# Performance work log

Measured on AMD Instinct MI355X. Metric: run time of the kernel, lower is better.

The kernel has to match this reference:

```python
import jax, jax.numpy as jnp
import numpy as np

N = 50000      # nodes
E = 800000     # edges
D_IN = 128
D_H = 256
D_OUT = 128
EPS = 1e-5
SLOPE = 0.01   # LeakyReLU negative_slope


def setup_inputs() -> dict:
    key = jax.random.key(0)
    ks = jax.random.split(key, 24)
    inp = {}
    inp["x"] = jax.random.normal(ks[0], (N, D_IN), dtype=jnp.float32)
    inp["edge_index"] = jax.random.randint(ks[1], (2, E), 0, N, dtype=jnp.int32)
    dims = [(D_IN, D_H), (D_H, D_H), (D_H, D_H), (D_H, D_OUT)]
    for i, (di, do) in enumerate(dims, start=1):
        inp[f"W{i}"] = jax.random.normal(ks[4 * i - 2], (di, do), dtype=jnp.float32) / np.float32(np.sqrt(di))
        inp[f"b{i}"] = jnp.zeros((do,), dtype=jnp.float32)
        inp[f"g{i}"] = 1.0 + 0.1 * jax.random.normal(ks[4 * i - 1], (do,), dtype=jnp.float32)   # BN gamma
        inp[f"be{i}"] = 0.1 * jax.random.normal(ks[4 * i], (do,), dtype=jnp.float32)            # BN beta
    inp["ln_g"] = 1.0 + 0.1 * jax.random.normal(ks[18], (D_OUT,), dtype=jnp.float32)
    inp["ln_b"] = 0.1 * jax.random.normal(ks[19], (D_OUT,), dtype=jnp.float32)
    return inp


def _gcn_conv(x, W, b, src, dst, nisq):
    # PyG GCNConv: linear first, then sym-normalized aggregation with self-loops.
    xl = x @ W                                   # [N, do]
    coef = (nisq[src] * nisq[dst])[:, None]      # [E, 1]
    msg = xl[src] * coef                         # [E, do] gather
    agg = jax.ops.segment_sum(msg, dst, num_segments=N)  # scatter-add
    # self-loop contribution: deg^{-1/2}_i * deg^{-1/2}_i * xl_i
    return agg + xl * (nisq * nisq)[:, None] + b


def _bn(x, g, b):
    # BatchNorm1d, training-mode batch statistics (biased variance)
    m = jnp.mean(x, axis=0)
    v = jnp.var(x, axis=0)
    return (x - m) * jax.lax.rsqrt(v + EPS) * g + b


def _lrelu(x):
    return jnp.where(x >= 0, x, SLOPE * x)


def _layer_norm(x, g, b):
    m = jnp.mean(x, axis=-1, keepdims=True)
    v = jnp.var(x, axis=-1, keepdims=True)
    return (x - m) * jax.lax.rsqrt(v + EPS) * g + b


def reference(x, edge_index, W1, b1, g1, be1, W2, b2, g2, be2, W3, b3, g3, be3, W4, b4, g4, be4, ln_g, ln_b):
    src = edge_index[0]
    dst = edge_index[1]
    # degrees with self-loops (computed once, shared by all 4 convs)
    deg = jax.ops.segment_sum(jnp.ones((E,), dtype=x.dtype), dst, num_segments=N) + 1.0
    nisq = jax.lax.rsqrt(deg)  # deg >= 1 so safe

    identity = x  # input_dim == output_dim -> residual_fc is Identity
    h = _lrelu(_bn(_gcn_conv(x, W1, b1, src, dst, nisq), g1, be1))   # dropout = identity (eval)
    h = _lrelu(_bn(_gcn_conv(h, W2, b2, src, dst, nisq), g2, be2))
    h = _lrelu(_bn(_gcn_conv(h, W3, b3, src, dst, nisq), g3, be3))
    h = _gcn_conv(h, W4, b4, src, dst, nisq)
    h = h + identity
    return _layer_norm(_bn(h, g4, be4), ln_g, ln_b)
```

## Files before the change

kernel.cpp:

```cpp
#include <hip/hip_runtime.h>

#define N_NODES 50000
#define NPAD 50176
#define N_EDGES 800000
#define EPS_C 1e-5f
#define SLOPE_C 0.01f

typedef __attribute__((ext_vector_type(8))) short short8v;
typedef __attribute__((ext_vector_type(4))) float f32x4;

__device__ __forceinline__ unsigned short f2bf(float f) {
  unsigned u = __float_as_uint(f);
  u += 0x7fffu + ((u >> 16) & 1u);
  return (unsigned short)(u >> 16);
}
__device__ __forceinline__ unsigned packbf(float a, float b) {
  return (unsigned)f2bf(a) | ((unsigned)f2bf(b) << 16);
}
__device__ __forceinline__ float bflo(unsigned u) { return __uint_as_float(u << 16); }
__device__ __forceinline__ float bfhi(unsigned u) { return __uint_as_float(u & 0xffff0000u); }

__device__ __forceinline__ void gload16(const unsigned short* g, unsigned short* l) {
  __builtin_amdgcn_global_load_lds(
      (const __attribute__((address_space(1))) unsigned int*)g,
      (__attribute__((address_space(3))) unsigned int*)l, 16, 0, 0);
}

#define HGRID 3125
__global__ void hist_wcast_kernel(const int* __restrict__ dst, int* __restrict__ hist,
                                  const float* __restrict__ W1, const float* __restrict__ W2,
                                  const float* __restrict__ W3, const float* __restrict__ W4,
                                  unsigned short* __restrict__ Wt1, unsigned short* __restrict__ Wt2,
                                  unsigned short* __restrict__ Wt3, unsigned short* __restrict__ Wt4) {
  const int b = blockIdx.x;
  if (b < HGRID) {
    const int e = b * 256 + threadIdx.x;
    if (e < N_EDGES) atomicAdd(&hist[dst[e]], 1);
    return;
  }
  const int w = (b - HGRID) * 256 + threadIdx.x;
  if (w < 32768) {
    Wt1[(size_t)(w & 255) * 128 + (w >> 8)] = f2bf(W1[w]);
  } else if (w < 98304) {
    const int v = w - 32768;
    Wt2[(size_t)(v & 255) * 256 + (v >> 8)] = f2bf(W2[v]);
  } else if (w < 163840) {
    const int v = w - 98304;
    Wt3[(size_t)(v & 255) * 256 + (v >> 8)] = f2bf(W3[v]);
  } else {
    const int v = w - 163840;
    Wt4[(size_t)(v & 127) * 256 + (v >> 7)] = f2bf(W4[v]);
  }
}

__global__ __launch_bounds__(1024) void scan1_kernel(
    const int* __restrict__ hist, int* __restrict__ off, int* __restrict__ partial,
    float* __restrict__ nisq, int n) {
  __shared__ int tmp[1024];
  const int tid = threadIdx.x;
  const int i = blockIdx.x * 1024 + tid;
  const int v = (i < n) ? hist[i] : 0;
  tmp[tid] = v;
  __syncthreads();
  int x = v;
  for (int o = 1; o < 1024; o <<= 1) {
    const int y = (tid >= o) ? tmp[tid - o] : 0;
    __syncthreads();
    x += y;
    tmp[tid] = x;
    __syncthreads();
  }
  if (i < n) {
    off[i] = x - v;
    nisq[i] = rsqrtf((float)v + 1.0f);
  }
  if (tid == 1023) partial[blockIdx.x] = x;
}

#define SGRID 196
#define NBCH 49
__global__ void scan3f_kernel(int* __restrict__ off, int* __restrict__ cursor,
                              const int* __restrict__ partial,
                              const float* __restrict__ nisq, const float* __restrict__ x,
                              unsigned short* __restrict__ xs) {
  const int b = blockIdx.x;
  if (b < SGRID) {
    const int i = b * 256 + threadIdx.x;
    const int chunk = b >> 2;
    int pre = 0;
    for (int k = 0; k < chunk; ++k) pre += partial[k];
    if (i < N_NODES) {
      const int o = off[i] + pre;
      off[i] = o;
      cursor[i] = o;
    }
    if (b == SGRID - 1 && threadIdx.x == 0)
      off[N_NODES] = pre + partial[NBCH - 1];
    return;
  }
  const int idx = (b - SGRID) * 256 + threadIdx.x;
  if (idx >= N_NODES * 32) return;
  const int row = idx >> 5;
  const int c = (idx & 31) * 4;
  const float s = nisq[row];
  const float4 v = *reinterpret_cast<const float4*>(&x[(size_t)row * 128 + c]);
  ushort4 o;
  o.x = f2bf(v.x * s); o.y = f2bf(v.y * s);
  o.z = f2bf(v.z * s); o.w = f2bf(v.w * s);
  *reinterpret_cast<ushort4*>(&xs[(size_t)row * 128 + c]) = o;
}

__global__ void scatter_kernel(const int* __restrict__ src, const int* __restrict__ dst,
                               int* __restrict__ cursor, int* __restrict__ esorted, int E) {
  const int e = blockIdx.x * 256 + threadIdx.x;
  if (e < E) {
    const int p = atomicAdd(&cursor[dst[e]], 1);
    esorted[p] = src[e];
  }
}

template <int MODE, int KC, int NCOL_LOG2>
__global__ __launch_bounds__(256) void gemm2_kernel(
    const unsigned short* __restrict__ A, const unsigned short* __restrict__ Wt,
    const float* __restrict__ bias, unsigned short* __restrict__ Yb,
    float* __restrict__ colsum, float* __restrict__ colsumsq, int M) {
  __shared__ __align__(16) unsigned short Bs[64][KC];
  __shared__ __align__(16) unsigned short As[128][64];
  __shared__ float sred[2][64][2];
  const int tid = threadIdx.x;
  const int lane = tid & 63;
  const int wave = tid >> 6;
  const int wr = wave >> 1, wc = wave & 1;
  const int chunkN = gridDim.x >> 3;
  const int swz = (blockIdx.x & 7) * chunkN + (blockIdx.x >> 3);
  const int row0 = (swz >> NCOL_LOG2) * 128;
  const int col0 = (swz & ((1 << NCOL_LOG2) - 1)) * 64;
  const int l15 = lane & 15;
  const int lhi = lane >> 4;

  constexpr int CPR = KC / 8;
  constexpr int BITER = 64 * CPR / 256;
#pragma unroll
  for (int c = 0; c < BITER; ++c) {
    const int ch = c * 256 + tid;
    const int rb = ch / CPR;
    const int cb = ch % CPR;
    const short8v v =
        *reinterpret_cast<const short8v*>(&Wt[(size_t)(col0 + rb) * KC + cb * 8]);
    *reinterpret_cast<short8v*>(&Bs[rb][(cb ^ (rb & 7)) * 8]) = v;
  }

  f32x4 acc[4][2];
#pragma unroll
  for (int i = 0; i < 4; ++i)
#pragma unroll
    for (int j = 0; j < 2; ++j) acc[i][j] = (f32x4){0.f, 0.f, 0.f, 0.f};

  for (int k0 = 0; k0 < KC; k0 += 64) {
    __syncthreads();
#pragma unroll
    for (int c = 0; c < 4; ++c) {
      const int chunk = (c * 4 + wave) * 64 + lane;
      const int r = chunk >> 3;
      const int cksrc = (chunk & 7) ^ (r & 7);
      gload16(&A[(size_t)(row0 + r) * KC + k0 + cksrc * 8], &As[0][0] + chunk * 8);
    }
    __syncthreads();
    short8v bfr[2][2];
#pragma unroll
    for (int nr = 0; nr < 2; ++nr)
#pragma unroll
      for (int h = 0; h < 2; ++h) {
        const int rowb = wc * 32 + nr * 16 + l15;
        const int chb = (k0 >> 3) + h * 4 + lhi;
        bfr[nr][h] = *reinterpret_cast<const short8v*>(&Bs[rowb][(chb ^ (rowb & 7)) * 8]);
      }
#pragma unroll
    for (int mr = 0; mr < 4; ++mr) {
#pragma unroll
      for (int h = 0; h < 2; ++h) {
        const int rowa = wr * 64 + mr * 16 + l15;
        const int cha = (h * 4 + lhi) ^ (rowa & 7);
        const short8v af = *reinterpret_cast<const short8v*>(&As[rowa][cha * 8]);
#pragma unroll
        for (int nr = 0; nr < 2; ++nr)
          acc[mr][nr] = __builtin_amdgcn_mfma_f32_16x16x32_bf16(
              af, bfr[nr][h], acc[mr][nr], 0, 0, 0);
      }
    }
  }
  float bcol[2] = {0.f, 0.f};
  if constexpr (MODE == 1) {
#pragma unroll
    for (int nr = 0; nr < 2; ++nr) bcol[nr] = bias[col0 + wc * 32 + nr * 16 + l15];
  }
  float s_c[2] = {0.f, 0.f}, q_c[2] = {0.f, 0.f};
#pragma unroll
  for (int mr = 0; mr < 4; ++mr) {
#pragma unroll
    for (int r = 0; r < 4; ++r) {
      const int grow = row0 + wr * 64 + mr * 16 + lhi * 4 + r;
#pragma unroll
      for (int nr = 0; nr < 2; ++nr) {
        const int gcol = col0 + wc * 32 + nr * 16 + l15;
        const float v = acc[mr][nr][r] + bcol[nr];
        Yb[(size_t)grow * M + gcol] = f2bf(v);
        if constexpr (MODE == 1) {
          if (grow < N_NODES) {
            s_c[nr] += v;
            q_c[nr] += v * v;
          }
        }
      }
    }
  }
  if constexpr (MODE == 1) {
#pragma unroll
    for (int nr = 0; nr < 2; ++nr) {
      float s = s_c[nr], q = q_c[nr];
      s += __shfl_xor(s, 16, 64); q += __shfl_xor(q, 16, 64);
      s += __shfl_xor(s, 32, 64); q += __shfl_xor(q, 32, 64);
      if (lhi == 0) {
        const int cl = wc * 32 + nr * 16 + l15;
        sred[0][cl][wr] = s;
        sred[1][cl][wr] = q;
      }
    }
    __syncthreads();
    if (tid < 128) {
      const int which = tid >> 6;
      const int cl = tid & 63;
      const float tot = sred[which][cl][0] + sred[which][cl][1];
      float* dstp = which ? colsumsq : colsum;
      atomicAdd(&dstp[col0 + cl], tot);
    }
  }
}

template <int DO, bool ADD_BIAS, bool HAS_RES, bool OUT_BF16>
__global__ __launch_bounds__(256) void aggregate4_kernel(
    const unsigned short* __restrict__ Y, const int* __restrict__ segoff,
    const int* __restrict__ esorted, const float* __restrict__ nisq,
    const float* __restrict__ bias, const float* __restrict__ resid,
    void* __restrict__ Tv) {
  constexpr int V2 = DO / 32;
  const int wave = threadIdx.x >> 6;
  const int lane = threadIdx.x & 63;
  const int half = lane >> 5;
  const int l31 = lane & 31;
  const int n = blockIdx.x * 4 + wave;
  const int colbase = l31 * V2;
  if (n >= N_NODES) {
    if (half == 0) {
      if constexpr (OUT_BF16) {
        unsigned short* tr = (unsigned short*)Tv + (size_t)n * DO + colbase;
        if constexpr (V2 == 8) *reinterpret_cast<uint4*>(tr) = (uint4){0, 0, 0, 0};
        else *reinterpret_cast<uint2*>(tr) = (uint2){0, 0};
      } else {
        float* tr = (float*)Tv + (size_t)n * DO + colbase;
        if constexpr (V2 == 8) {
          *reinterpret_cast<float4*>(tr) = (float4){0.f, 0.f, 0.f, 0.f};
          *reinterpret_cast<float4*>(tr + 4) = (float4){0.f, 0.f, 0.f, 0.f};
        } else {
          *reinterpret_cast<float4*>(tr) = (float4){0.f, 0.f, 0.f, 0.f};
        }
      }
    }
    return;
  }
  const unsigned short* Yc = Y + colbase;
  float a0[V2], a1[V2];
#pragma unroll
  for (int i = 0; i < V2; ++i) { a0[i] = 0.f; a1[i] = 0.f; }
  const int s = segoff[n];
  const int e = segoff[n + 1];

  if constexpr (V2 == 8) {
    auto acc8 = [&](float* a, const uint4 v) {
      a[0] += bflo(v.x); a[1] += bfhi(v.x);
      a[2] += bflo(v.y); a[3] += bfhi(v.y);
      a[4] += bflo(v.z); a[5] += bfhi(v.z);
      a[6] += bflo(v.w); a[7] += bfhi(v.w);
    };
    int j = s + half;
    for (; j + 2 < e; j += 4) {
      const int i0 = esorted[j];
      const int i1 = esorted[j + 2];
      const uint4 v0 = *reinterpret_cast<const uint4*>(Yc + (size_t)i0 * DO);
      const uint4 v1 = *reinterpret_cast<const uint4*>(Yc + (size_t)i1 * DO);
      acc8(a0, v0); acc8(a1, v1);
    }
    if (j < e) acc8(a0, *reinterpret_cast<const uint4*>(Yc + (size_t)esorted[j] * DO));
    if (half == 0) acc8(a1, *reinterpret_cast<const uint4*>(Yc + (size_t)n * DO));
  } else {
    auto acc4 = [&](float* a, const uint2 v) {
      a[0] += bflo(v.x); a[1] += bfhi(v.x);
      a[2] += bflo(v.y); a[3] += bfhi(v.y);
    };
    int j = s + half;
    for (; j + 2 < e; j += 4) {
      const int i0 = esorted[j];
      const int i1 = esorted[j + 2];
      const uint2 v0 = *reinterpret_cast<const uint2*>(Yc + (size_t)i0 * DO);
      const uint2 v1 = *reinterpret_cast<const uint2*>(Yc + (size_t)i1 * DO);
      acc4(a0, v0); acc4(a1, v1);
    }
    if (j < e) acc4(a0, *reinterpret_cast<const uint2*>(Yc + (size_t)esorted[j] * DO));
    if (half == 0) acc4(a1, *reinterpret_cast<const uint2*>(Yc + (size_t)n * DO));
  }

  const float sc = nisq[n];
  float vals[V2];
#pragma unroll
  for (int i = 0; i < V2; ++i) {
    float t = a0[i] + a1[i];
    t += __shfl_xor(t, 32, 64);
    t *= sc;
    if (half == 0) {
      if (ADD_BIAS) t += bias[colbase + i];
      if (HAS_RES) t += resid[(size_t)n * DO + colbase + i];
    }
    vals[i] = t;
  }
  if (half == 0) {
    if constexpr (OUT_BF16) {
      unsigned short* tr = (unsigned short*)Tv + (size_t)n * DO + colbase;
      if constexpr (V2 == 8) {
        uint4 o;
        o.x = packbf(vals[0], vals[1]); o.y = packbf(vals[2], vals[3]);
        o.z = packbf(vals[4], vals[5]); o.w = packbf(vals[6], vals[7]);
        *reinterpret_cast<uint4*>(tr) = o;
      } else {
        uint2 o;
        o.x = packbf(vals[0], vals[1]); o.y = packbf(vals[2], vals[3]);
        *reinterpret_cast<uint2*>(tr) = o;
      }
    } else {
      float* tr = (float*)Tv + (size_t)n * DO + colbase;
      if constexpr (V2 == 8) {
        float4 o0 = {vals[0], vals[1], vals[2], vals[3]};
        float4 o1 = {vals[4], vals[5], vals[6], vals[7]};
        *reinterpret_cast<float4*>(tr) = o0;
        *reinterpret_cast<float4*>(tr + 4) = o1;
      } else {
        float4 o = {vals[0], vals[1], vals[2], vals[3]};
        *reinterpret_cast<float4*>(tr) = o;
      }
    }
  }
}

__global__ void stats_bf16_kernel(const unsigned short* __restrict__ T,
                                  float* __restrict__ colsum, float* __restrict__ colsumsq,
                                  int n, int rowsPerBlock) {
  const int t = threadIdx.x;
  const int c2 = t & 63;
  const int rh = t >> 6;
  const int r0 = blockIdx.x * rowsPerBlock;
  int r1 = r0 + rowsPerBlock;
  if (r1 > n) r1 = n;
  const unsigned* T32 = (const unsigned*)T;
  float s0 = 0.f, q0 = 0.f, s1 = 0.f, q1 = 0.f;
  for (int r = r0 + rh; r < r1; r += 2) {
    const unsigned v = T32[(size_t)r * 64 + c2];
    const float a = bflo(v), b = bfhi(v);
    s0 += a; q0 += a * a;
    s1 += b; q1 += b * b;
  }
  atomicAdd(&colsum[c2 * 2], s0);
  atomicAdd(&colsumsq[c2 * 2], q0);
  atomicAdd(&colsum[c2 * 2 + 1], s1);
  atomicAdd(&colsumsq[c2 * 2 + 1], q1);
}

__global__ void bn_lrelu_nisq_kernel(const unsigned short* __restrict__ Tb,
                                     const float* __restrict__ colsum,
                                     const float* __restrict__ colsumsq,
                                     const float* __restrict__ g, const float* __restrict__ be,
                                     const float* __restrict__ nisq,
                                     unsigned short* __restrict__ outb,
                                     size_t total8, float invN) {
  const size_t idx = (size_t)blockIdx.x * 256 + threadIdx.x;
  if (idx >= total8) return;
  const int row = (int)(idx >> 5);
  if (row >= N_NODES) {
    *reinterpret_cast<uint4*>(&outb[idx * 8]) = (uint4){0, 0, 0, 0};
    return;
  }
  const unsigned c = ((unsigned)idx & 31u) * 8;
  const float sc = nisq[row];
  uint4 v = *reinterpret_cast<const uint4*>(&Tb[idx * 8]);
  float z[8] = {bflo(v.x), bfhi(v.x), bflo(v.y), bfhi(v.y),
                bflo(v.z), bfhi(v.z), bflo(v.w), bfhi(v.w)};
  const float4 cs0 = *reinterpret_cast<const float4*>(&colsum[c]);
  const float4 cs1 = *reinterpret_cast<const float4*>(&colsum[c + 4]);
  const float4 cq0 = *reinterpret_cast<const float4*>(&colsumsq[c]);
  const float4 cq1 = *reinterpret_cast<const float4*>(&colsumsq[c + 4]);
  const float4 gv0 = *reinterpret_cast<const float4*>(&g[c]);
  const float4 gv1 = *reinterpret_cast<const float4*>(&g[c + 4]);
  const float4 bv0 = *reinterpret_cast<const float4*>(&be[c]);
  const float4 bv1 = *reinterpret_cast<const float4*>(&be[c + 4]);
  const float css[8] = {cs0.x, cs0.y, cs0.z, cs0.w, cs1.x, cs1.y, cs1.z, cs1.w};
  const float cqq[8] = {cq0.x, cq0.y, cq0.z, cq0.w, cq1.x, cq1.y, cq1.z, cq1.w};
  const float ggg[8] = {gv0.x, gv0.y, gv0.z, gv0.w, gv1.x, gv1.y, gv1.z, gv1.w};
  const float bbb[8] = {bv0.x, bv0.y, bv0.z, bv0.w, bv1.x, bv1.y, bv1.z, bv1.w};
#pragma unroll
  for (int k = 0; k < 8; ++k) {
    const float m = css[k] * invN;
    const float rs = rsqrtf(cqq[k] * invN - m * m + EPS_C);
    float zz = (z[k] - m) * rs * ggg[k] + bbb[k];
    zz = (zz >= 0.f) ? zz : SLOPE_C * zz;
    z[k] = zz * sc;
  }
  v.x = packbf(z[0], z[1]); v.y = packbf(z[2], z[3]);
  v.z = packbf(z[4], z[5]); v.w = packbf(z[6], z[7]);
  *reinterpret_cast<uint4*>(&outb[idx * 8]) = v;
}

__global__ __launch_bounds__(256) void bn_ln_kernel(
    const unsigned short* __restrict__ T, const float* __restrict__ colsum,
    const float* __restrict__ colsumsq, const float* __restrict__ g,
    const float* __restrict__ be, const float* __restrict__ lng,
    const float* __restrict__ lnb, float* __restrict__ out, float invN) {
  const int wave = threadIdx.x >> 6;
  const int lane = threadIdx.x & 63;
  const int n = blockIdx.x * 4 + wave;
  if (n >= N_NODES) return;
  const int c = lane * 2;
  const unsigned tv = *reinterpret_cast<const unsigned*>(&T[(size_t)n * 128 + c]);
  const float t0 = bflo(tv), t1 = bfhi(tv);
  float z[2];
#pragma unroll
  for (int k = 0; k < 2; ++k) {
    const float m = colsum[c + k] * invN;
    const float v = colsumsq[c + k] * invN - m * m;
    const float tvv = (k == 0) ? t0 : t1;
    z[k] = (tvv - m) * rsqrtf(v + EPS_C) * g[c + k] + be[c + k];
  }
  float s = z[0] + z[1];
  float q = z[0] * z[0] + z[1] * z[1];
  for (int o = 32; o > 0; o >>= 1) {
    s += __shfl_xor(s, o, 64);
    q += __shfl_xor(q, o, 64);
  }
  const float mean = s * (1.f / 128.f);
  const float var = q * (1.f / 128.f) - mean * mean;
  const float rs = rsqrtf(var + EPS_C);
  float2 o2;
  o2.x = (z[0] - mean) * rs * lng[c] + lnb[c];
  o2.y = (z[1] - mean) * rs * lng[c + 1] + lnb[c + 1];
  *reinterpret_cast<float2*>(&out[(size_t)n * 128 + c]) = o2;
}

extern "C" void kernel_launch(void* const* d_in, const int* in_sizes, int n_in,
                              void* d_out, int out_size, void* d_ws, size_t ws_size,
                              hipStream_t stream) {
  const float* x = (const float*)d_in[0];
  const int* ei = (const int*)d_in[1];
  const int* srcp = ei;
  const int* dstp = ei + N_EDGES;
  const float* W1 = (const float*)d_in[2];
  const float* b1 = (const float*)d_in[3];
  const float* g1 = (const float*)d_in[4];
  const float* be1 = (const float*)d_in[5];
  const float* W2 = (const float*)d_in[6];
  const float* b2 = (const float*)d_in[7];
  const float* g2 = (const float*)d_in[8];
  const float* be2 = (const float*)d_in[9];
  const float* W3 = (const float*)d_in[10];
  const float* b3 = (const float*)d_in[11];
  const float* g3 = (const float*)d_in[12];
  const float* be3 = (const float*)d_in[13];
  const float* W4 = (const float*)d_in[14];
  const float* b4 = (const float*)d_in[15];
  const float* g4 = (const float*)d_in[16];
  const float* be4 = (const float*)d_in[17];
  const float* lng = (const float*)d_in[18];
  const float* lnb = (const float*)d_in[19];
  float* out = (float*)d_out;

  char* ws = (char*)d_ws;
  size_t off_b = 0;
  auto alloc = [&](size_t bytes) -> void* {
    void* p = (void*)(ws + off_b);
    off_b += (bytes + 255) & ~(size_t)255;
    return p;
  };
  int* hist = (int*)alloc((size_t)N_NODES * 4);
  float* cs1 = (float*)alloc(256 * 4);
  float* cq1 = (float*)alloc(256 * 4);
  float* cs2 = (float*)alloc(256 * 4);
  float* cq2 = (float*)alloc(256 * 4);
  float* cs3 = (float*)alloc(256 * 4);
  float* cq3 = (float*)alloc(256 * 4);
  float* cs4 = (float*)alloc(256 * 4);
  float* cq4 = (float*)alloc(256 * 4);
  const size_t zero_bytes = off_b;
  int* segoff = (int*)alloc((size_t)(N_NODES + 1) * 4);
  int* cursor = (int*)alloc((size_t)N_NODES * 4);
  float* nisq = (float*)alloc((size_t)N_NODES * 4);
  int* esorted = (int*)alloc((size_t)N_EDGES * 4);
  int* partial = (int*)alloc(64 * 4);
  unsigned short* Wt1 = (unsigned short*)alloc((size_t)256 * 128 * 2);
  unsigned short* Wt2 = (unsigned short*)alloc((size_t)256 * 256 * 2);
  unsigned short* Wt3 = (unsigned short*)alloc((size_t)256 * 256 * 2);
  unsigned short* Wt4 = (unsigned short*)alloc((size_t)128 * 256 * 2);
  unsigned short* tblA = (unsigned short*)alloc((size_t)NPAD * 256 * 2);
  unsigned short* tblB = (unsigned short*)alloc((size_t)NPAD * 256 * 2);
  unsigned short* S = (unsigned short*)alloc((size_t)NPAD * 256 * 2);
  unsigned short* Tb = (unsigned short*)alloc((size_t)NPAD * 256 * 2);

  const float invN = 1.0f / (float)N_NODES;
  const int egrid = (N_EDGES + 255) / 256;
  const int aggrid = NPAD / 4;
  const int statgrid = (N_NODES + 127) / 128;
  const int mgrid256 = (NPAD / 128) * 4;
  const int mgrid128 = (NPAD / 128) * 2;
  const unsigned bngrid = (unsigned)(((size_t)NPAD * 32 + 255) / 256);

  hipMemsetAsync(hist, 0, zero_bytes, stream);

  hist_wcast_kernel<<<HGRID + 768, 256, 0, stream>>>(dstp, hist, W1, W2, W3, W4,
                                                     Wt1, Wt2, Wt3, Wt4);
  scan1_kernel<<<NBCH, 1024, 0, stream>>>(hist, segoff, partial, nisq, N_NODES);
  scan3f_kernel<<<SGRID + 6250, 256, 0, stream>>>(segoff, cursor, partial, nisq, x, tblA);
  scatter_kernel<<<egrid, 256, 0, stream>>>(srcp, dstp, cursor, esorted, N_EDGES);

  aggregate4_kernel<128, false, false, true><<<aggrid, 256, 0, stream>>>(
      tblA, segoff, esorted, nisq, nullptr, nullptr, S);
  gemm2_kernel<1, 128, 2><<<mgrid256, 256, 0, stream>>>(S, Wt1, b1, Tb, cs1, cq1, 256);
  bn_lrelu_nisq_kernel<<<bngrid, 256, 0, stream>>>(Tb, cs1, cq1, g1, be1, nisq,
                                                   tblB, (size_t)NPAD * 32, invN);

  aggregate4_kernel<256, false, false, true><<<aggrid, 256, 0, stream>>>(
      tblB, segoff, esorted, nisq, nullptr, nullptr, S);
  gemm2_kernel<1, 256, 2><<<mgrid256, 256, 0, stream>>>(S, Wt2, b2, Tb, cs2, cq2, 256);
  bn_lrelu_nisq_kernel<<<bngrid, 256, 0, stream>>>(Tb, cs2, cq2, g2, be2, nisq,
                                                   tblA, (size_t)NPAD * 32, invN);

  aggregate4_kernel<256, false, false, true><<<aggrid, 256, 0, stream>>>(
      tblA, segoff, esorted, nisq, nullptr, nullptr, S);
  gemm2_kernel<1, 256, 2><<<mgrid256, 256, 0, stream>>>(S, Wt3, b3, Tb, cs3, cq3, 256);
  bn_lrelu_nisq_kernel<<<bngrid, 256, 0, stream>>>(Tb, cs3, cq3, g3, be3, nisq,
                                                   tblB, (size_t)NPAD * 32, invN);

  gemm2_kernel<0, 256, 1><<<mgrid128, 256, 0, stream>>>(tblB, Wt4, nullptr, S,
                                                        nullptr, nullptr, 128);
  aggregate4_kernel<128, true, true, true><<<aggrid, 256, 0, stream>>>(
      S, segoff, esorted, nisq, b4, x, Tb);
  stats_bf16_kernel<<<statgrid, 128, 0, stream>>>(Tb, cs4, cq4, N_NODES, 128);
  bn_ln_kernel<<<(N_NODES + 3) / 4, 256, 0, stream>>>(Tb, cs4, cq4, g4, be4, lng, lnb, out, invN);
}
```

Before: 478.4 us.

## Widen GEMM tile to 128x128 and stream weight slices per k-step via LDS

The GEMM kernel's output tile grows from 128x64 to 128x128, so each wave computes a 64x64 sub-tile with 16 accumulators. Instead of preloading the whole weight panel into shared memory up front, the 64-wide k-slice of the weights is loaded asynchronously through global_load_lds alongside A each k-step. This halves the number of blocks and the redundant A-tile reads across column tiles. In exchange it uses more registers per thread, and the smaller grid (about 784 or 392 blocks) may fill the GPU's compute units less evenly.

```diff
diff --git a/kernel.cpp b/kernel.cpp
--- a/kernel.cpp
+++ b/kernel.cpp
@@ -120,13 +120,13 @@
 }
 
 template <int MODE, int KC, int NCOL_LOG2>
-__global__ __launch_bounds__(256) void gemm2_kernel(
+__global__ __launch_bounds__(256) void gemm4_kernel(
     const unsigned short* __restrict__ A, const unsigned short* __restrict__ Wt,
     const float* __restrict__ bias, unsigned short* __restrict__ Yb,
     float* __restrict__ colsum, float* __restrict__ colsumsq, int M) {
-  __shared__ __align__(16) unsigned short Bs[64][KC];
   __shared__ __align__(16) unsigned short As[128][64];
-  __shared__ float sred[2][64][2];
+  __shared__ __align__(16) unsigned short Bs[128][64];
+  __shared__ float sred[2][128][2];
   const int tid = threadIdx.x;
   const int lane = tid & 63;
   const int wave = tid >> 6;
@@ -134,27 +134,15 @@
   const int chunkN = gridDim.x >> 3;
   const int swz = (blockIdx.x & 7) * chunkN + (blockIdx.x >> 3);
   const int row0 = (swz >> NCOL_LOG2) * 128;
-  const int col0 = (swz & ((1 << NCOL_LOG2) - 1)) * 64;
+  const int col0 = (swz & ((1 << NCOL_LOG2) - 1)) * 128;
   const int l15 = lane & 15;
   const int lhi = lane >> 4;
 
-  constexpr int CPR = KC / 8;
-  constexpr int BITER = 64 * CPR / 256;
-#pragma unroll
-  for (int c = 0; c < BITER; ++c) {
-    const int ch = c * 256 + tid;
-    const int rb = ch / CPR;
-    const int cb = ch % CPR;
-    const short8v v =
-        *reinterpret_cast<const short8v*>(&Wt[(size_t)(col0 + rb) * KC + cb * 8]);
-    *reinterpret_cast<short8v*>(&Bs[rb][(cb ^ (rb & 7)) * 8]) = v;
-  }
-
-  f32x4 acc[4][2];
+  f32x4 acc[4][4];
 #pragma unroll
   for (int i = 0; i < 4; ++i)
 #pragma unroll
-    for (int j = 0; j < 2; ++j) acc[i][j] = (f32x4){0.f, 0.f, 0.f, 0.f};
+    for (int j = 0; j < 4; ++j) acc[i][j] = (f32x4){0.f, 0.f, 0.f, 0.f};
 
   for (int k0 = 0; k0 < KC; k0 += 64) {
     __syncthreads();
@@ -162,47 +150,52 @@
     for (int c = 0; c < 4; ++c) {
       const int chunk = (c * 4 + wave) * 64 + lane;
       const int r = chunk >> 3;
-      const int cksrc = (chunk & 7) ^ (r & 7);
-      gload16(&A[(size_t)(row0 + r) * KC + k0 + cksrc * 8], &As[0][0] + chunk * 8);
+      const int ck = (chunk & 7) ^ (r & 7);
+      gload16(&A[(size_t)(row0 + r) * KC + k0 + ck * 8], &As[0][0] + chunk * 8);
+    }
+#pragma unroll
+    for (int c = 0; c < 4; ++c) {
+      const int chunk = (c * 4 + wave) * 64 + lane;
+      const int r = chunk >> 3;
+      const int ck = (chunk & 7) ^ (r & 7);
+      gload16(&Wt[(size_t)(col0 + r) * KC + k0 + ck * 8], &Bs[0][0] + chunk * 8);
     }
     __syncthreads();
-    short8v bfr[2][2];
-#pragma unroll
-    for (int nr = 0; nr < 2; ++nr)
-#pragma unroll
-      for (int h = 0; h < 2; ++h) {
-        const int rowb = wc * 32 + nr * 16 + l15;
-        const int chb = (k0 >> 3) + h * 4 + lhi;
-        bfr[nr][h] = *reinterpret_cast<const short8v*>(&Bs[rowb][(chb ^ (rowb & 7)) * 8]);
-      }
-#pragma unroll
-    for (int mr = 0; mr < 4; ++mr) {
-#pragma unroll
-      for (int h = 0; h < 2; ++h) {
+#pragma unroll
+    for (int h = 0; h < 2; ++h) {
+      short8v bfr[4];
+#pragma unroll
+      for (int nr = 0; nr < 4; ++nr) {
+        const int rowb = wc * 64 + nr * 16 + l15;
+        const int chb = (h * 4 + lhi) ^ (rowb & 7);
+        bfr[nr] = *reinterpret_cast<const short8v*>(&Bs[rowb][chb * 8]);
+      }
+#pragma unroll
+      for (int mr = 0; mr < 4; ++mr) {
         const int rowa = wr * 64 + mr * 16 + l15;
         const int cha = (h * 4 + lhi) ^ (rowa & 7);
         const short8v af = *reinterpret_cast<const short8v*>(&As[rowa][cha * 8]);
 #pragma unroll
-        for (int nr = 0; nr < 2; ++nr)
+        for (int nr = 0; nr < 4; ++nr)
           acc[mr][nr] = __builtin_amdgcn_mfma_f32_16x16x32_bf16(
-              af, bfr[nr][h], acc[mr][nr], 0, 0, 0);
-      }
-    }
-  }
-  float bcol[2] = {0.f, 0.f};
+              af, bfr[nr], acc[mr][nr], 0, 0, 0);
+      }
+    }
+  }
+  float bcol[4] = {0.f, 0.f, 0.f, 0.f};
   if constexpr (MODE == 1) {
 #pragma unroll
-    for (int nr = 0; nr < 2; ++nr) bcol[nr] = bias[col0 + wc * 32 + nr * 16 + l15];
-  }
-  float s_c[2] = {0.f, 0.f}, q_c[2] = {0.f, 0.f};
+    for (int nr = 0; nr < 4; ++nr) bcol[nr] = bias[col0 + wc * 64 + nr * 16 + l15];
+  }
+  float s_c[4] = {0.f, 0.f, 0.f, 0.f}, q_c[4] = {0.f, 0.f, 0.f, 0.f};
 #pragma unroll
   for (int mr = 0; mr < 4; ++mr) {
 #pragma unroll
     for (int r = 0; r < 4; ++r) {
       const int grow = row0 + wr * 64 + mr * 16 + lhi * 4 + r;
 #pragma unroll
-      for (int nr = 0; nr < 2; ++nr) {
-        const int gcol = col0 + wc * 32 + nr * 16 + l15;
+      for (int nr = 0; nr < 4; ++nr) {
+        const int gcol = col0 + wc * 64 + nr * 16 + l15;
         const float v = acc[mr][nr][r] + bcol[nr];
         Yb[(size_t)grow * M + gcol] = f2bf(v);
         if constexpr (MODE == 1) {
@@ -216,20 +209,20 @@
   }
   if constexpr (MODE == 1) {
 #pragma unroll
-    for (int nr = 0; nr < 2; ++nr) {
+    for (int nr = 0; nr < 4; ++nr) {
       float s = s_c[nr], q = q_c[nr];
       s += __shfl_xor(s, 16, 64); q += __shfl_xor(q, 16, 64);
       s += __shfl_xor(s, 32, 64); q += __shfl_xor(q, 32, 64);
       if (lhi == 0) {
-        const int cl = wc * 32 + nr * 16 + l15;
+        const int cl = wc * 64 + nr * 16 + l15;
         sred[0][cl][wr] = s;
         sred[1][cl][wr] = q;
       }
     }
     __syncthreads();
-    if (tid < 128) {
-      const int which = tid >> 6;
-      const int cl = tid & 63;
+    {
+      const int which = tid >> 7;
+      const int cl = tid & 127;
       const float tot = sred[which][cl][0] + sred[which][cl][1];
       float* dstp = which ? colsumsq : colsum;
       atomicAdd(&dstp[col0 + cl], tot);
@@ -514,8 +507,8 @@
   const int egrid = (N_EDGES + 255) / 256;
   const int aggrid = NPAD / 4;
   const int statgrid = (N_NODES + 127) / 128;
-  const int mgrid256 = (NPAD / 128) * 4;
-  const int mgrid128 = (NPAD / 128) * 2;
+  const int mgrid256 = (NPAD / 128) * 2;
+  const int mgrid128 = (NPAD / 128);
   const unsigned bngrid = (unsigned)(((size_t)NPAD * 32 + 255) / 256);
 
   hipMemsetAsync(hist, 0, zero_bytes, stream);
@@ -528,23 +521,23 @@
 
   aggregate4_kernel<128, false, false, true><<<aggrid, 256, 0, stream>>>(
       tblA, segoff, esorted, nisq, nullptr, nullptr, S);
-  gemm2_kernel<1, 128, 2><<<mgrid256, 256, 0, stream>>>(S, Wt1, b1, Tb, cs1, cq1, 256);
+  gemm4_kernel<1, 128, 1><<<mgrid256, 256, 0, stream>>>(S, Wt1, b1, Tb, cs1, cq1, 256);
   bn_lrelu_nisq_kernel<<<bngrid, 256, 0, stream>>>(Tb, cs1, cq1, g1, be1, nisq,
                                                    tblB, (size_t)NPAD * 32, invN);
 
   aggregate4_kernel<256, false, false, true><<<aggrid, 256, 0, stream>>>(
       tblB, segoff, esorted, nisq, nullptr, nullptr, S);
-  gemm2_kernel<1, 256, 2><<<mgrid256, 256, 0, stream>>>(S, Wt2, b2, Tb, cs2, cq2, 256);
+  gemm4_kernel<1, 256, 1><<<mgrid256, 256, 0, stream>>>(S, Wt2, b2, Tb, cs2, cq2, 256);
   bn_lrelu_nisq_kernel<<<bngrid, 256, 0, stream>>>(Tb, cs2, cq2, g2, be2, nisq,
                                                    tblA, (size_t)NPAD * 32, invN);
 
   aggregate4_kernel<256, false, false, true><<<aggrid, 256, 0, stream>>>(
       tblA, segoff, esorted, nisq, nullptr, nullptr, S);
-  gemm2_kernel<1, 256, 2><<<mgrid256, 256, 0, stream>>>(S, Wt3, b3, Tb, cs3, cq3, 256);
+  gemm4_kernel<1, 256, 1><<<mgrid256, 256, 0, stream>>>(S, Wt3, b3, Tb, cs3, cq3, 256);
   bn_lrelu_nisq_kernel<<<bngrid, 256, 0, stream>>>(Tb, cs3, cq3, g3, be3, nisq,
                                                    tblB, (size_t)NPAD * 32, invN);
 
-  gemm2_kernel<0, 256, 1><<<mgrid128, 256, 0, stream>>>(tblB, Wt4, nullptr, S,
+  gemm4_kernel<0, 256, 0><<<mgrid128, 256, 0, stream>>>(tblB, Wt4, nullptr, S,
                                                         nullptr, nullptr, 128);
   aggregate4_kernel<128, true, true, true><<<aggrid, 256, 0, stream>>>(
       S, segoff, esorted, nisq, b4, x, Tb);
```

New measurement: 483.7 us. No clear change (+1.1%).
